# Optimization experiments

Measured on AMD Instinct MI355X. Metric: run time of the kernel, lower is better.

## Reference

```python
import jax, jax.numpy as jnp
import numpy as np

TEMPERATURE = 0.5
EPS = 1e-8  # torch cosine_similarity norm clamp


def setup_inputs() -> dict:
    key = jax.random.key(0)
    k1, k2, k3 = jax.random.split(key, 3)
    N, D = 4096, 256
    z_i = jax.random.normal(k1, (N, D), dtype=jnp.float32)
    z_j = jax.random.normal(k2, (N, D), dtype=jnp.float32)
    weights = jax.random.uniform(k3, (N,), dtype=jnp.float32)
    return {"z_i": z_i, "z_j": z_j, "weights": weights}


def reference(z_i, z_j, weights):
    N = z_i.shape[0]
    z = jnp.concatenate([z_i, z_j], axis=0)  # [2N, D]
    # cosine similarity via normalized matmul (same math as broadcasted F.cosine_similarity)
    norm = jnp.maximum(jnp.linalg.norm(z, axis=1, keepdims=True), EPS)
    zn = z / norm
    sim = zn @ zn.T  # [2N, 2N]
    # positives: diagonals at offsets +N and -N
    sim_ij = jnp.diagonal(sim, offset=N)
    sim_ji = jnp.diagonal(sim, offset=-N)
    positives = jnp.concatenate([sim_ij, sim_ji], axis=0)  # [2N]
    mask = 1.0 - jnp.eye(2 * N, dtype=sim.dtype)
    denominator = jnp.sum(mask * jnp.exp(sim / TEMPERATURE), axis=1)  # [2N]
    numerator = jnp.exp(positives / TEMPERATURE)
    all_losses = -jnp.log(numerator / denominator)  # [2N]
    w2 = jnp.tile(weights, 2)  # weights.repeat(2)
    loss = jnp.sum(all_losses * w2) / jnp.sum(w2)
    return loss
```

## Files before the change

kernel.cpp:

```cpp
#include <hip/hip_runtime.h>
#include <hip/hip_bf16.h>

#define PN   4096
#define PN2  8192
#define PD   256
#define TILE 128
#define BK   64

typedef __attribute__((ext_vector_type(8))) short bf16x8;
typedef __attribute__((ext_vector_type(4))) float f32x4;

typedef const __attribute__((address_space(1))) void* gas_ptr;
typedef __attribute__((address_space(3))) void* las_ptr;

__global__ __launch_bounds__(256) void normalize_kernel(
    const float* __restrict__ zi, const float* __restrict__ zj,
    __hip_bfloat16* __restrict__ zn, float* __restrict__ rowsum) {
  int r = blockIdx.x;
  int tid = threadIdx.x;
  const float* src = (r < PN) ? (zi + (size_t)r * PD) : (zj + (size_t)(r - PN) * PD);
  float x = src[tid];
  float s = x * x;
  #pragma unroll
  for (int off = 32; off >= 1; off >>= 1) s += __shfl_xor(s, off, 64);
  __shared__ float p[4];
  if ((tid & 63) == 0) p[tid >> 6] = s;
  __syncthreads();
  float tot = p[0] + p[1] + p[2] + p[3];
  float nrm = fmaxf(sqrtf(tot), 1e-8f);
  zn[(size_t)r * PD + tid] = __float2bfloat16(x / nrm);
  if (tid == 0) rowsum[r] = 0.0f;
}

__global__ __launch_bounds__(256) void simsum_kernel(
    const __hip_bfloat16* __restrict__ zn,
    float* __restrict__ rowsum, float* __restrict__ pos) {
  __shared__ char lds[2 * TILE * BK * 2];
  char* As = lds;
  char* Bs = lds + TILE * BK * 2;

  const int tid  = threadIdx.x;
  const int wave = tid >> 6;
  const int lane = tid & 63;
  const int quad = lane >> 4;
  const int c16  = lane & 15;
  const int rowBase = blockIdx.x * TILE;
  const int colBase = blockIdx.y * TILE;
  const int waveRow = (wave >> 1) * 64;
  const int waveCol = (wave & 1) * 64;

  f32x4 acc[4][4];
  #pragma unroll
  for (int i = 0; i < 4; ++i)
    #pragma unroll
    for (int j = 0; j < 4; ++j)
      acc[i][j] = (f32x4){0.f, 0.f, 0.f, 0.f};

  const int subrow = lane >> 3;
  const int slot   = lane & 7;

  for (int kt = 0; kt < PD / BK; ++kt) {
    if (kt) __syncthreads();
    #pragma unroll
    for (int p = 0; p < 4; ++p) {
      int issue = wave * 4 + p;
      int r = issue * 8 + subrow;
      int c = slot ^ (r & 7);
      const __hip_bfloat16* ga = zn + (size_t)(rowBase + r) * PD + kt * BK + c * 8;
      __builtin_amdgcn_global_load_lds((gas_ptr)ga, (las_ptr)(As + issue * 1024), 16, 0, 0);
      const __hip_bfloat16* gb = zn + (size_t)(colBase + r) * PD + kt * BK + c * 8;
      __builtin_amdgcn_global_load_lds((gas_ptr)gb, (las_ptr)(Bs + issue * 1024), 16, 0, 0);
    }
    __syncthreads();

    #pragma unroll
    for (int ki = 0; ki < 2; ++ki) {
      bf16x8 a[4], b[4];
      #pragma unroll
      for (int mi = 0; mi < 4; ++mi) {
        int r = waveRow + mi * 16 + c16;
        int ch = quad + ki * 4;
        a[mi] = *(const bf16x8*)(As + r * 128 + ((ch ^ (r & 7)) * 16));
      }
      #pragma unroll
      for (int ni = 0; ni < 4; ++ni) {
        int r = waveCol + ni * 16 + c16;
        int ch = quad + ki * 4;
        b[ni] = *(const bf16x8*)(Bs + r * 128 + ((ch ^ (r & 7)) * 16));
      }
      #pragma unroll
      for (int mi = 0; mi < 4; ++mi)
        #pragma unroll
        for (int ni = 0; ni < 4; ++ni)
          acc[mi][ni] = __builtin_amdgcn_mfma_f32_16x16x32_bf16(a[mi], b[ni], acc[mi][ni], 0, 0, 0);
    }
  }

  #pragma unroll
  for (int mi = 0; mi < 4; ++mi) {
    int rbase = rowBase + waveRow + mi * 16 + quad * 4;
    float rs[4] = {0.f, 0.f, 0.f, 0.f};
    #pragma unroll
    for (int ni = 0; ni < 4; ++ni) {
      int gcol = colBase + waveCol + ni * 16 + c16;
      #pragma unroll
      for (int t = 0; t < 4; ++t) {
        int grow = rbase + t;
        float sim = acc[mi][ni][t];
        if (gcol == (grow ^ PN)) pos[grow] = sim;
        rs[t] += (gcol == grow) ? 0.0f : __expf(2.0f * sim);
      }
    }
    #pragma unroll
    for (int t = 0; t < 4; ++t) {
      #pragma unroll
      for (int off = 1; off <= 8; off <<= 1) rs[t] += __shfl_xor(rs[t], off, 64);
    }
    if (c16 == 0) {
      #pragma unroll
      for (int t = 0; t < 4; ++t) atomicAdd(&rowsum[rbase + t], rs[t]);
    }
  }
}

__global__ __launch_bounds__(256) void finalize_kernel(
    const float* __restrict__ rowsum, const float* __restrict__ pos,
    const float* __restrict__ w, float* __restrict__ out) {
  int tid = threadIdx.x;
  float wl = 0.f, ws = 0.f;
  for (int i = tid; i < PN2; i += 256) {
    float li = logf(rowsum[i]) - 2.0f * pos[i];
    float wi = w[i & (PN - 1)];
    wl += wi * li;
    ws += wi;
  }
  #pragma unroll
  for (int off = 32; off >= 1; off >>= 1) {
    wl += __shfl_xor(wl, off, 64);
    ws += __shfl_xor(ws, off, 64);
  }
  __shared__ float pl[4], pw[4];
  if ((tid & 63) == 0) { pl[tid >> 6] = wl; pw[tid >> 6] = ws; }
  __syncthreads();
  if (tid == 0)
    out[0] = (pl[0] + pl[1] + pl[2] + pl[3]) / (pw[0] + pw[1] + pw[2] + pw[3]);
}

extern "C" void kernel_launch(void* const* d_in, const int* in_sizes, int n_in,
                              void* d_out, int out_size, void* d_ws, size_t ws_size,
                              hipStream_t stream) {
  const float* zi = (const float*)d_in[0];
  const float* zj = (const float*)d_in[1];
  const float* w  = (const float*)d_in[2];
  float* out = (float*)d_out;

  __hip_bfloat16* zn = (__hip_bfloat16*)d_ws;
  float* rowsum = (float*)((char*)d_ws + (size_t)PN2 * PD * 2);
  float* pos = rowsum + PN2;

  normalize_kernel<<<PN2, 256, 0, stream>>>(zi, zj, zn, rowsum);
  dim3 grid(PN2 / TILE, PN2 / TILE);
  simsum_kernel<<<grid, 256, 0, stream>>>(zn, rowsum, pos);
  finalize_kernel<<<1, 256, 0, stream>>>(rowsum, pos, w, out);
}
```

Before: 128.5 us.

## Exploit similarity matrix symmetry by computing only upper-triangular tiles

Launches only the upper-triangular set of 128x128 tiles, decoding (bi,bj) from a linear block index, and adds each off-diagonal tile's exp values both to row sums and, through column reductions, to the mirrored rows' sums. Diagonal tiles load one operand and reuse it for both sides, and positive-pair similarities are written for both halves from the single off-diagonal tile. This roughly halves the MFMA and exp work at the cost of more atomics per tile and some index arithmetic. The finalize kernel also moves to 1024 threads.

```diff
diff --git a/kernel.cpp b/kernel.cpp
--- a/kernel.cpp
+++ b/kernel.cpp
@@ -6,6 +6,8 @@
 #define PD   256
 #define TILE 128
 #define BK   64
+#define NBLK (PN2 / TILE)
+#define NTRI (NBLK * (NBLK + 1) / 2)
 
 typedef __attribute__((ext_vector_type(8))) short bf16x8;
 typedef __attribute__((ext_vector_type(4))) float f32x4;
@@ -39,13 +41,21 @@
   char* As = lds;
   char* Bs = lds + TILE * BK * 2;
 
+  const int idx = blockIdx.x;
+  int bj = (int)((sqrtf(8.0f * (float)idx + 1.0f) - 1.0f) * 0.5f);
+  while ((bj + 1) * (bj + 2) / 2 <= idx) ++bj;
+  while (bj * (bj + 1) / 2 > idx) --bj;
+  const int bi = idx - bj * (bj + 1) / 2;
+  const bool diagBlk = (bi == bj);
+  const bool posBlk  = (bj == bi + PN / TILE);
+
   const int tid  = threadIdx.x;
   const int wave = tid >> 6;
   const int lane = tid & 63;
   const int quad = lane >> 4;
   const int c16  = lane & 15;
-  const int rowBase = blockIdx.x * TILE;
-  const int colBase = blockIdx.y * TILE;
+  const int rowBase = bi * TILE;
+  const int colBase = bj * TILE;
   const int waveRow = (wave >> 1) * 64;
   const int waveCol = (wave & 1) * 64;
 
@@ -58,6 +68,7 @@
 
   const int subrow = lane >> 3;
   const int slot   = lane & 7;
+  const char* BsEff = diagBlk ? As : Bs;
 
   for (int kt = 0; kt < PD / BK; ++kt) {
     if (kt) __syncthreads();
@@ -68,8 +79,10 @@
       int c = slot ^ (r & 7);
       const __hip_bfloat16* ga = zn + (size_t)(rowBase + r) * PD + kt * BK + c * 8;
       __builtin_amdgcn_global_load_lds((gas_ptr)ga, (las_ptr)(As + issue * 1024), 16, 0, 0);
-      const __hip_bfloat16* gb = zn + (size_t)(colBase + r) * PD + kt * BK + c * 8;
-      __builtin_amdgcn_global_load_lds((gas_ptr)gb, (las_ptr)(Bs + issue * 1024), 16, 0, 0);
+      if (!diagBlk) {
+        const __hip_bfloat16* gb = zn + (size_t)(colBase + r) * PD + kt * BK + c * 8;
+        __builtin_amdgcn_global_load_lds((gas_ptr)gb, (las_ptr)(Bs + issue * 1024), 16, 0, 0);
+      }
     }
     __syncthreads();
 
@@ -86,7 +99,7 @@
       for (int ni = 0; ni < 4; ++ni) {
         int r = waveCol + ni * 16 + c16;
         int ch = quad + ki * 4;
-        b[ni] = *(const bf16x8*)(Bs + r * 128 + ((ch ^ (r & 7)) * 16));
+        b[ni] = *(const bf16x8*)(BsEff + r * 128 + ((ch ^ (r & 7)) * 16));
       }
       #pragma unroll
       for (int mi = 0; mi < 4; ++mi)
@@ -96,6 +109,7 @@
     }
   }
 
+  float colsum[4] = {0.f, 0.f, 0.f, 0.f};
   #pragma unroll
   for (int mi = 0; mi < 4; ++mi) {
     int rbase = rowBase + waveRow + mi * 16 + quad * 4;
@@ -107,8 +121,14 @@
       for (int t = 0; t < 4; ++t) {
         int grow = rbase + t;
         float sim = acc[mi][ni][t];
-        if (gcol == (grow ^ PN)) pos[grow] = sim;
-        rs[t] += (gcol == grow) ? 0.0f : __expf(2.0f * sim);
+        float e = __expf(2.0f * sim);
+        if (diagBlk && gcol == grow) e = 0.0f;
+        rs[t] += e;
+        colsum[ni] += e;
+        if (posBlk && gcol == grow + PN) {
+          pos[grow] = sim;
+          pos[grow + PN] = sim;
+        }
       }
     }
     #pragma unroll
@@ -121,14 +141,23 @@
       for (int t = 0; t < 4; ++t) atomicAdd(&rowsum[rbase + t], rs[t]);
     }
   }
+  if (!diagBlk) {
+    #pragma unroll
+    for (int ni = 0; ni < 4; ++ni) {
+      float cs = colsum[ni];
+      cs += __shfl_xor(cs, 16, 64);
+      cs += __shfl_xor(cs, 32, 64);
+      if (quad == 0) atomicAdd(&rowsum[colBase + waveCol + ni * 16 + c16], cs);
+    }
+  }
 }
 
-__global__ __launch_bounds__(256) void finalize_kernel(
+__global__ __launch_bounds__(1024) void finalize_kernel(
     const float* __restrict__ rowsum, const float* __restrict__ pos,
     const float* __restrict__ w, float* __restrict__ out) {
   int tid = threadIdx.x;
   float wl = 0.f, ws = 0.f;
-  for (int i = tid; i < PN2; i += 256) {
+  for (int i = tid; i < PN2; i += 1024) {
     float li = logf(rowsum[i]) - 2.0f * pos[i];
     float wi = w[i & (PN - 1)];
     wl += wi * li;
@@ -139,11 +168,15 @@
     wl += __shfl_xor(wl, off, 64);
     ws += __shfl_xor(ws, off, 64);
   }
-  __shared__ float pl[4], pw[4];
+  __shared__ float pl[16], pw[16];
   if ((tid & 63) == 0) { pl[tid >> 6] = wl; pw[tid >> 6] = ws; }
   __syncthreads();
-  if (tid == 0)
-    out[0] = (pl[0] + pl[1] + pl[2] + pl[3]) / (pw[0] + pw[1] + pw[2] + pw[3]);
+  if (tid == 0) {
+    float sl = 0.f, sw = 0.f;
+    #pragma unroll
+    for (int k = 0; k < 16; ++k) { sl += pl[k]; sw += pw[k]; }
+    out[0] = sl / sw;
+  }
 }
 
 extern "C" void kernel_launch(void* const* d_in, const int* in_sizes, int n_in,
@@ -159,7 +192,6 @@
   float* pos = rowsum + PN2;
 
   normalize_kernel<<<PN2, 256, 0, stream>>>(zi, zj, zn, rowsum);
-  dim3 grid(PN2 / TILE, PN2 / TILE);
-  simsum_kernel<<<grid, 256, 0, stream>>>(zn, rowsum, pos);
-  finalize_kernel<<<1, 256, 0, stream>>>(rowsum, pos, w, out);
+  simsum_kernel<<<NTRI, 256, 0, stream>>>(zn, rowsum, pos);
+  finalize_kernel<<<1, 1024, 0, stream>>>(rowsum, pos, w, out);
 }
```

Result: faster. 108.6 us (-15.4%).
